# Kernel tuning notes

Hardware: AMD Instinct MI355X
Metric: run time of the kernel (lower is better)

## Reference

```python
import jax, jax.numpy as jnp
import numpy as np

# dimensions
N = 50000    # nodes
E = 600000   # edges
NS = 64      # scalar (0e) channels of node features
NV = 32      # vector (1o) channels of node features
A = 16       # node attr channels (16x0e)
R = 8        # edge embedding dim (radial basis, 8x0e)
H = 8        # fc_hidden_size
AVG_NB = 12.0  # avg_num_neighbors
# gate layout: NS scalars (silu) + NV gate scalars (sigmoid) gating NV vectors
GS = NS + NV  # 96 scalar channels before gate
NW = NS + NS + NV + NV  # 192 per-edge TP weights (paths: s*Y0->0e, s*Y1->1o, v*Y0->1o, v.Y1->0e)


def setup_inputs() -> dict:
    key = jax.random.key(0)
    ks = jax.random.split(key, 20)
    d = {
        'node_s': jax.random.normal(ks[0], (N, NS), jnp.float32),
        'node_v': jax.random.normal(ks[1], (N, NV, 3), jnp.float32),
        'node_attrs': jax.random.normal(ks[2], (N, A), jnp.float32),
        'edge_emb': jax.random.uniform(ks[3], (E, R), jnp.float32),
        'edge_sh0': jnp.ones((E, 1), jnp.float32),
        'edge_sh1': jax.random.normal(ks[4], (E, 3), jnp.float32),
        'edge_index': jax.random.randint(ks[5], (2, E), 0, N),
        # linear_1 on node feats (per-irrep channel mixing)
        'W1s': jax.random.normal(ks[6], (NS, NS), jnp.float32),
        'W1v': jax.random.normal(ks[7], (NV, NV), jnp.float32),
        # radial MLP producing per-edge TP weights
        'Wm1': jax.random.normal(ks[8], (R, H), jnp.float32),
        'Wm2': jax.random.normal(ks[9], (H, NW), jnp.float32),
        # linear_2: TP out (96x0e+96x1o) -> pre-gate (96x0e+32x1o)
        'W2s': jax.random.normal(ks[10], (GS, GS), jnp.float32),
        'W2v': jax.random.normal(ks[11], (NS + NV, NV), jnp.float32),
        # update UVU TP internal weights (msg x attrs)
        'Wt0': jax.random.normal(ks[12], (NS, A), jnp.float32),
        'Wt1': jax.random.normal(ks[13], (NV, A), jnp.float32),
        # linear_3
        'W3s': jax.random.normal(ks[14], (NS, GS), jnp.float32),
        'W3v': jax.random.normal(ks[15], (NV, NV), jnp.float32),
        # self connection: FullyConnectedTensorProduct(node_feats, attrs -> pre-gate)
        'Wsc0': jax.random.normal(ks[16], (NS, A, GS), jnp.float32),
        'Wsc1': jax.random.normal(ks[17], (NV, A, NV), jnp.float32),
    }
    return d


def _gate(s_all, v):
    # s_all: [.., GS]; first NS scalars -> silu, last NV -> sigmoid gates for vectors
    scal = jax.nn.silu(s_all[..., :NS])
    gates = jax.nn.sigmoid(s_all[..., NS:])
    return scal, v * gates[..., None]


def reference(node_s, node_v, node_attrs, edge_emb, edge_sh0, edge_sh1, edge_index,
              W1s, W1v, Wm1, Wm2, W2s, W2v, Wt0, Wt1, W3s, W3v, Wsc0, Wsc1):
    src, dst = edge_index[0], edge_index[1]

    # ---- message ----
    s1 = (node_s @ W1s) / jnp.sqrt(jnp.float32(NS))                       # [N,NS]
    v1 = jnp.einsum('nuc,uv->nvc', node_v, W1v) / jnp.sqrt(jnp.float32(NV))
    ss = s1[src]   # [E,NS]
    vv = v1[src]   # [E,NV,3]

    # per-edge TP weights from radial MLP
    w = jax.nn.silu(edge_emb @ Wm1) @ Wm2                                 # [E,NW]
    w0a, w1a, w1b, w0b = jnp.split(w, [NS, 2 * NS, 2 * NS + NV], axis=1)

    # UVU tensor product with SH edge attrs (lmax=1)
    t0a = w0a * ss * edge_sh0                                             # [E,NS] 0e
    t0b = w0b * jnp.einsum('euc,ec->eu', vv, edge_sh1)                    # [E,NV] 0e
    t1a = w1a[:, :, None] * ss[:, :, None] * edge_sh1[:, None, :]         # [E,NS,3] 1o
    t1b = w1b[:, :, None] * vv * edge_sh0[:, :, None]                     # [E,NV,3] 1o
    tp_s = jnp.concatenate([t0a, t0b], axis=1)                            # [E,96]
    tp_v = jnp.concatenate([t1a, t1b], axis=1)                            # [E,96,3]

    m_s = (tp_s @ W2s) / jnp.sqrt(jnp.float32(GS))                        # [E,GS]
    m_v = jnp.einsum('euc,uv->evc', tp_v, W2v) / jnp.sqrt(jnp.float32(NS + NV))  # [E,NV,3]
    msg_s, msg_v = _gate(m_s, m_v)                                        # [E,NS], [E,NV,3]

    # ---- update ----
    agg_s = jax.ops.segment_sum(msg_s, dst, num_segments=N) / jnp.sqrt(jnp.float32(AVG_NB))
    agg_v = jax.ops.segment_sum(msg_v, dst, num_segments=N) / jnp.sqrt(jnp.float32(AVG_NB))

    u0 = jnp.einsum('nu,na,ua->nu', agg_s, node_attrs, Wt0) / jnp.sqrt(jnp.float32(A))
    u1 = jnp.einsum('nuc,na,ua->nuc', agg_v, node_attrs, Wt1) / jnp.sqrt(jnp.float32(A))

    f_s = (u0 @ W3s) / jnp.sqrt(jnp.float32(NS))                          # [N,GS]
    f_v = jnp.einsum('nuc,uv->nvc', u1, W3v) / jnp.sqrt(jnp.float32(NV))  # [N,NV,3]

    # self connection (fully connected TP with scalar attrs)
    sc_s = jnp.einsum('nu,na,uav->nv', node_s, node_attrs, Wsc0) / jnp.sqrt(jnp.float32(NS * A))
    sc_v = jnp.einsum('nuc,na,uaw->nwc', node_v, node_attrs, Wsc1) / jnp.sqrt(jnp.float32(NV * A))
    f_s = f_s + sc_s
    f_v = f_v + sc_v

    out_s, out_v = _gate(f_s, f_v)                                        # [N,NS], [N,NV,3]
    return jnp.concatenate([out_s, out_v.reshape(N, NV * 3)], axis=1)     # [N,160]
```

## Files before the change

kernel.cpp:

```cpp
#include <hip/hip_runtime.h>
#include <math.h>

#define N 50000
#define E 600000
#define EPB 16
#define LDK 104

typedef __attribute__((ext_vector_type(8))) short short8;
typedef __attribute__((ext_vector_type(4))) float float4v;

__device__ __forceinline__ float silu_f(float x) { return x / (1.f + __expf(-x)); }
__device__ __forceinline__ float sigm_f(float x) { return 1.f / (1.f + __expf(-x)); }
__device__ __forceinline__ unsigned short f2bf(float f) {
  unsigned u = __float_as_uint(f);
  u += 0x7fff + ((u >> 16) & 1);
  return (unsigned short)(u >> 16);
}
__device__ __forceinline__ float bf2f(unsigned short u) {
  return __uint_as_float(((unsigned)u) << 16);
}

__global__ void k_hist(const int* __restrict__ eidx, int* __restrict__ counts) {
  int e = blockIdx.x * 256 + threadIdx.x;
  if (e < E) atomicAdd(&counts[eidx[E + e]], 1);
}

__global__ __launch_bounds__(1024)
void k_scan(const int* __restrict__ counts, int* __restrict__ row_ptr) {
  __shared__ int ssum[1024];
  const int t = threadIdx.x;
  const int CH = 49;
  int lo = t * CH, hi = min(lo + CH, N);
  int s = 0;
  for (int i = lo; i < hi; i++) s += counts[i];
  ssum[t] = s;
  __syncthreads();
  for (int off = 1; off < 1024; off <<= 1) {
    int v = (t >= off) ? ssum[t - off] : 0;
    __syncthreads();
    ssum[t] += v;
    __syncthreads();
  }
  int run = (t == 0) ? 0 : ssum[t - 1];
  for (int i = lo; i < hi; i++) { row_ptr[i] = run; run += counts[i]; }
  if (t == 1023) row_ptr[N] = ssum[1023];
}

__global__ void k_scatter(const int* __restrict__ eidx, const int* __restrict__ row_ptr,
                          int* __restrict__ woff, int* __restrict__ perm) {
  int e = blockIdx.x * 256 + threadIdx.x;
  if (e < E) {
    int d = eidx[E + e];
    int p = atomicAdd(&woff[d], 1);
    perm[row_ptr[d] + p] = e;
  }
}

__global__ void k_prep(const float* __restrict__ Wsc0, const float* __restrict__ W3s,
                       const float* __restrict__ Wsc1, const float* __restrict__ W3v,
                       const float* __restrict__ W2s, const float* __restrict__ W2v,
                       unsigned short* __restrict__ BT, unsigned short* __restrict__ B2T,
                       unsigned short* __restrict__ w2sTg, unsigned short* __restrict__ w2vTg) {
  const float isq96 = 0.10206207261596575f;
  int i = blockIdx.x * 256 + threadIdx.x;
  if (i < 96 * 1088) {
    int j = i / 1088, k = i % 1088;
    float v;
    if (k < 1024) v = Wsc0[(size_t)k * 96 + j] * 0.03125f;
    else          v = W3s[(size_t)(k - 1024) * 96 + j] * 0.125f;
    BT[i] = f2bf(v);
  } else if (i < 96 * 1088 + 32 * 576) {
    int i2 = i - 96 * 1088;
    int w = i2 / 576, k = i2 % 576;
    float v = 0.f;
    if (k < 512)      v = Wsc1[(size_t)k * 32 + w] * 0.04419417382415922f;
    else if (k < 544) v = W3v[(size_t)(k - 512) * 32 + w] * 0.17677669529663689f;
    B2T[i2] = f2bf(v);
  } else if (i < 96 * 1088 + 32 * 576 + 96 * 96) {
    int i3 = i - (96 * 1088 + 32 * 576);
    int j = i3 / 96, k = i3 % 96;
    w2sTg[i3] = f2bf(W2s[(size_t)k * 96 + j] * isq96);
  } else {
    int i4 = i - (96 * 1088 + 32 * 576 + 96 * 96);
    if (i4 < 32 * 96) {
      int v = i4 / 96, u = i4 % 96;
      w2vTg[i4] = f2bf(W2v[(size_t)u * 32 + v] * isq96);
    }
  }
}

__global__ __launch_bounds__(256, 4)
void k_lin1(const float* __restrict__ node_s, const float* __restrict__ node_v,
            const float* __restrict__ W1s, const float* __restrict__ W1v,
            float* __restrict__ s1, float* __restrict__ v1) {
  __shared__ float w1s[64 * 64];
  __shared__ float w1v[32 * 32];
  for (int i = threadIdx.x; i < 64 * 64; i += 256) w1s[i] = W1s[i];
  for (int i = threadIdx.x; i < 32 * 32; i += 256) w1v[i] = W1v[i];
  __syncthreads();
  const float is_ns = 0.125f;
  const float is_nv = 0.17677669529663689f;
  int gtid = blockIdx.x * 256 + threadIdx.x;
  int stride = gridDim.x * 256;
  for (int i = gtid; i < N * 160; i += stride) {
    int n = i / 160, ch = i % 160;
    if (ch < 64) {
      const float* row = node_s + n * 64;
      float acc = 0.f;
#pragma unroll
      for (int u = 0; u < 64; u++) acc += row[u] * w1s[u * 64 + ch];
      s1[n * 64 + ch] = acc * is_ns;
    } else {
      int p = ch - 64, v = p / 3, c = p % 3;
      const float* row = node_v + n * 96;
      float acc = 0.f;
#pragma unroll
      for (int u = 0; u < 32; u++) acc += row[u * 3 + c] * w1v[u * 32 + v];
      v1[n * 96 + p] = acc * is_nv;
    }
  }
}

template<int STORE>
__global__ __launch_bounds__(256, 4)
void k_msg(const float* __restrict__ s1, const float* __restrict__ v1,
           const float* __restrict__ emb, const float* __restrict__ sh0g,
           const float* __restrict__ sh1g, const int* __restrict__ eidx,
           const int* __restrict__ perm,
           const float* __restrict__ Wm1, const float* __restrict__ Wm2,
           const unsigned short* __restrict__ w2sTg, const unsigned short* __restrict__ w2vTg,
           float* __restrict__ aggs, float* __restrict__ aggv,
           unsigned short* __restrict__ msgS, unsigned short* __restrict__ msgV) {
  __shared__ float wm2s[192 * 9];
  __shared__ float wm1s[64];
  __shared__ unsigned short tps[EPB * LDK];
  __shared__ unsigned short tpv[EPB * 3 * LDK];
  __shared__ float gat[EPB][33];
  __shared__ float hb[EPB][8];
  __shared__ float sh1b[EPB][4];
  __shared__ float sh0b[EPB];
  __shared__ int ssrc[EPB];
  __shared__ int sdst[EPB];

  const int t = threadIdx.x;
  const int wave = t >> 6, lane = t & 63;
  const int lm = lane & 15, quad = lane >> 4;
  const int subc = t & 15;

  for (int i = t; i < 192 * 8; i += 256) {
    int h = i / 192, c = i % 192;
    wm2s[c * 9 + h] = Wm2[i];
  }
  if (t < 64) wm1s[t] = Wm1[t];

  short8 b1fr[2][3], b2fr[3];
  {
    const int nt0 = wave;
    const int nt1 = (wave + 4 < 6) ? wave + 4 : wave;
    const int nv2 = wave & 1;
#pragma unroll
    for (int kk = 0; kk < 3; kk++) {
      b1fr[0][kk] = *(const short8*)&w2sTg[(nt0 * 16 + lm) * 96 + kk * 32 + quad * 8];
      b1fr[1][kk] = *(const short8*)&w2sTg[(nt1 * 16 + lm) * 96 + kk * 32 + quad * 8];
      b2fr[kk]    = *(const short8*)&w2vTg[(nv2 * 16 + lm) * 96 + kk * 32 + quad * 8];
    }
  }
  __syncthreads();

  for (int pass = blockIdx.x; pass < E / EPB; pass += gridDim.x) {
    const int ebase = pass * EPB;
    __syncthreads();
    if (t < EPB) {
      const int e = STORE ? perm[ebase + t] : (ebase + t);
      ssrc[t] = eidx[e];
      if (!STORE) sdst[t] = eidx[E + ebase + t];
      sh0b[t] = sh0g[e];
    } else if (t >= 64 && t < 64 + EPB * 3) {
      int i = t - 64;
      const int el = i / 3, c = i % 3;
      const int e = STORE ? perm[ebase + el] : (ebase + el);
      sh1b[el][c] = sh1g[e * 3 + c];
    } else if (t >= 128) {
      int i = t - 128, el = i >> 3, sub = i & 7;
      const int e = STORE ? perm[ebase + el] : (ebase + el);
      float acc = 0.f;
#pragma unroll
      for (int r = 0; r < 8; r++) acc += emb[e * 8 + r] * wm1s[r * 8 + sub];
      hb[el][sub] = silu_f(acc);
    }
    __syncthreads();
    {
      const int el = t >> 4, sub = subc;
      const int src = ssrc[el];
      const float s0v = sh0b[el];
      const float x0 = sh1b[el][0], x1 = sh1b[el][1], x2 = sh1b[el][2];
      float hr[8];
#pragma unroll
      for (int h = 0; h < 8; h++) hr[h] = hb[el][h];
      const float4v ss = *(const float4v*)&s1[(size_t)src * 64 + sub * 4];
      unsigned short tsv[4], tvv[3][4];
#pragma unroll
      for (int i = 0; i < 4; i++) {
        float w0a = 0.f, w1a = 0.f;
#pragma unroll
        for (int h = 0; h < 8; h++) {
          w0a += hr[h] * wm2s[(sub * 4 + i) * 9 + h];
          w1a += hr[h] * wm2s[(64 + sub * 4 + i) * 9 + h];
        }
        const float ssu = ss[i];
        tsv[i] = f2bf(w0a * ssu * s0v);
        const float base = w1a * ssu;
        tvv[0][i] = f2bf(base * x0);
        tvv[1][i] = f2bf(base * x1);
        tvv[2][i] = f2bf(base * x2);
      }
      *(uint2*)&tps[el * LDK + sub * 4] = *(uint2*)tsv;
#pragma unroll
      for (int c = 0; c < 3; c++)
        *(uint2*)&tpv[(el * 3 + c) * LDK + sub * 4] = *(uint2*)tvv[c];
      const float2* vp = (const float2*)&v1[(size_t)src * 96 + sub * 6];
      const float2 va = vp[0], vb = vp[1], vc = vp[2];
      const float v6[6] = {va.x, va.y, vb.x, vb.y, vc.x, vc.y};
      unsigned short ts2[2], tv2[3][2];
#pragma unroll
      for (int i2 = 0; i2 < 2; i2++) {
        float w1b = 0.f, w0b = 0.f;
#pragma unroll
        for (int h = 0; h < 8; h++) {
          w1b += hr[h] * wm2s[(128 + sub * 2 + i2) * 9 + h];
          w0b += hr[h] * wm2s[(160 + sub * 2 + i2) * 9 + h];
        }
        const float vx = v6[i2 * 3 + 0], vy = v6[i2 * 3 + 1], vz = v6[i2 * 3 + 2];
        ts2[i2] = f2bf(w0b * (vx * x0 + vy * x1 + vz * x2));
        tv2[0][i2] = f2bf(w1b * vx * s0v);
        tv2[1][i2] = f2bf(w1b * vy * s0v);
        tv2[2][i2] = f2bf(w1b * vz * s0v);
      }
      *(unsigned*)&tps[el * LDK + 64 + sub * 2] = *(unsigned*)ts2;
#pragma unroll
      for (int c = 0; c < 3; c++)
        *(unsigned*)&tpv[(el * 3 + c) * LDK + 64 + sub * 2] = *(unsigned*)tv2[c];
    }
    __syncthreads();
    {
      short8 afr[3];
#pragma unroll
      for (int kk = 0; kk < 3; kk++)
        afr[kk] = *(const short8*)&tps[lm * LDK + kk * 32 + quad * 8];
#pragma unroll
      for (int t2 = 0; t2 < 2; t2++) {
        const int nt = wave + t2 * 4;
        if (nt < 6) {
          float4v acc = {0.f, 0.f, 0.f, 0.f};
#pragma unroll
          for (int kk = 0; kk < 3; kk++)
            acc = __builtin_amdgcn_mfma_f32_16x16x32_bf16(afr[kk], b1fr[t2][kk], acc, 0, 0, 0);
          const int j = nt * 16 + lm;
#pragma unroll
          for (int reg = 0; reg < 4; reg++) {
            const int e = quad * 4 + reg;
            const float val = acc[reg];
            if (j < 64) {
              if (STORE) msgS[(size_t)(ebase + e) * 64 + j] = f2bf(silu_f(val));
              else atomicAdd(&aggs[(size_t)sdst[e] * 64 + j], silu_f(val));
            } else {
              gat[e][j - 64] = sigm_f(val);
            }
          }
        }
      }
    }
    __syncthreads();
#pragma unroll
    for (int t2 = 0; t2 < 2; t2++) {
      const int tile = wave + t2 * 4;
      if (tile < 6) {
        const int mt = tile >> 1, nt2 = tile & 1;
        float4v acc = {0.f, 0.f, 0.f, 0.f};
#pragma unroll
        for (int kk = 0; kk < 3; kk++) {
          short8 a = *(const short8*)&tpv[(mt * 16 + lm) * LDK + kk * 32 + quad * 8];
          acc = __builtin_amdgcn_mfma_f32_16x16x32_bf16(a, b2fr[kk], acc, 0, 0, 0);
        }
        const int v = nt2 * 16 + lm;
#pragma unroll
        for (int reg = 0; reg < 4; reg++) {
          const int r = mt * 16 + quad * 4 + reg;
          const int e = (r * 171) >> 9, c = r - 3 * e;
          const float val = acc[reg] * gat[e][v];
          if (STORE) msgV[(size_t)(ebase + e) * 96 + v * 3 + c] = f2bf(val);
          else atomicAdd(&aggv[(size_t)sdst[e] * 96 + v * 3 + c], val);
        }
      }
    }
  }
}

__global__ __launch_bounds__(256, 8)
void k_agg(const unsigned short* __restrict__ msgS, const unsigned short* __restrict__ msgV,
           const int* __restrict__ rowp,
           float* __restrict__ aggs, float* __restrict__ aggv) {
  const int wv = threadIdx.x >> 6, lane = threadIdx.x & 63;
  const int n = blockIdx.x * 4 + wv;
  const int lo = rowp[n], hi = rowp[n + 1];
  float sS = 0.f, v0 = 0.f, v1a = 0.f;
  int r = lo;
  for (; r + 2 <= hi; r += 2) {
    const unsigned short a0 = msgS[(size_t)r * 64 + lane];
    const unsigned short a1 = msgS[(size_t)(r + 1) * 64 + lane];
    const unsigned short b0 = msgV[(size_t)r * 96 + lane];
    const unsigned short b1 = msgV[(size_t)(r + 1) * 96 + lane];
    unsigned short c0 = 0, c1 = 0;
    if (lane < 32) {
      c0 = msgV[(size_t)r * 96 + 64 + lane];
      c1 = msgV[(size_t)(r + 1) * 96 + 64 + lane];
    }
    sS += bf2f(a0) + bf2f(a1);
    v0 += bf2f(b0) + bf2f(b1);
    v1a += bf2f(c0) + bf2f(c1);
  }
  for (; r < hi; r++) {
    sS += bf2f(msgS[(size_t)r * 64 + lane]);
    v0 += bf2f(msgV[(size_t)r * 96 + lane]);
    if (lane < 32) v1a += bf2f(msgV[(size_t)r * 96 + 64 + lane]);
  }
  aggs[(size_t)n * 64 + lane] = sS;
  aggv[(size_t)n * 96 + lane] = v0;
  if (lane < 32) aggv[(size_t)n * 96 + 64 + lane] = v1a;
}

__global__ __launch_bounds__(256, 4)
void k_c1(const float* __restrict__ node_s, const float* __restrict__ attrs,
          const float* __restrict__ aggs, const float* __restrict__ Wt0,
          const unsigned short* __restrict__ BT,
          float* __restrict__ out, float* __restrict__ gates) {
  __shared__ float s_row[32][64];
  __shared__ float attr[32][16];
  __shared__ float t0[32][64];
  __shared__ float wt0[1024];
  __shared__ unsigned short As[32 * 72];
  const int t = threadIdx.x;
  const int wave = t >> 6, lane = t & 63, lm = lane & 15, quad = lane >> 4;
  const int nbase = blockIdx.x * 32;

  for (int i = t; i < 1024; i += 256) wt0[i] = Wt0[i];
  for (int i = t; i < 2048; i += 256) {
    int nl = i >> 6, u = i & 63, n = nbase + nl;
    s_row[nl][u] = (n < N) ? node_s[(size_t)n * 64 + u] : 0.f;
    t0[nl][u]    = (n < N) ? aggs[(size_t)n * 64 + u] : 0.f;
  }
  for (int i = t; i < 512; i += 256) {
    int nl = i >> 4, a = i & 15, n = nbase + nl;
    attr[nl][a] = (n < N) ? attrs[(size_t)n * 16 + a] : 0.f;
  }
  __syncthreads();
  for (int i = t; i < 2048; i += 256) {
    int nl = i >> 6, u = i & 63;
    float d0 = 0.f;
#pragma unroll
    for (int a = 0; a < 16; a++) d0 += attr[nl][a] * wt0[u * 16 + a];
    t0[nl][u] *= d0 * 0.07216878364870322f;
  }

  float4v acc[3] = {{0,0,0,0},{0,0,0,0},{0,0,0,0}};
  int mts[3], nts[3];
#pragma unroll
  for (int tt = 0; tt < 3; tt++) {
    const int tile = wave + tt * 4;
    mts[tt] = tile / 6;
    nts[tt] = tile % 6;
  }

  for (int kc = 0; kc < 17; kc++) {
    __syncthreads();
    {
      const int row = t >> 3, c0 = (t & 7) * 8;
      unsigned short tmp[8];
      if (kc < 16) {
        const int u = kc * 4 + (c0 >> 4);
        const float sval = s_row[row][u];
        const int ab = c0 & 8;
#pragma unroll
        for (int i = 0; i < 8; i++) tmp[i] = f2bf(sval * attr[row][ab + i]);
      } else {
#pragma unroll
        for (int i = 0; i < 8; i++) tmp[i] = f2bf(t0[row][c0 + i]);
      }
      *(uint4*)&As[row * 72 + c0] = *(uint4*)tmp;
    }
    __syncthreads();
#pragma unroll
    for (int ks = 0; ks < 2; ks++) {
      short8 am0 = *(const short8*)&As[(lm) * 72 + ks * 32 + quad * 8];
      short8 am1 = *(const short8*)&As[(16 + lm) * 72 + ks * 32 + quad * 8];
#pragma unroll
      for (int tt = 0; tt < 3; tt++) {
        short8 b = *(const short8*)&BT[(size_t)(nts[tt] * 16 + lm) * 1088 + kc * 64 + ks * 32 + quad * 8];
        acc[tt] = __builtin_amdgcn_mfma_f32_16x16x32_bf16(mts[tt] ? am1 : am0, b, acc[tt], 0, 0, 0);
      }
    }
  }
#pragma unroll
  for (int tt = 0; tt < 3; tt++) {
    const int j = nts[tt] * 16 + lm;
#pragma unroll
    for (int reg = 0; reg < 4; reg++) {
      const int m = mts[tt] * 16 + quad * 4 + reg;
      const int n = nbase + m;
      if (n < N) {
        const float val = acc[tt][reg];
        if (j < 64) out[(size_t)n * 160 + j] = silu_f(val);
        else        gates[(size_t)n * 32 + (j - 64)] = sigm_f(val);
      }
    }
  }
}

__global__ __launch_bounds__(256, 3)
void k_c2(const float* __restrict__ node_v, const float* __restrict__ attrs,
          const float* __restrict__ aggv, const float* __restrict__ Wt1,
          const unsigned short* __restrict__ B2T, const float* __restrict__ gts,
          float* __restrict__ out) {
  __shared__ float nvs[32][96];
  __shared__ float t1s[32][96];
  __shared__ float attr[32][16];
  __shared__ float wt1[512];
  __shared__ unsigned short As2[96 * 72];
  const int t = threadIdx.x;
  const int wave = t >> 6, lane = t & 63, lm = lane & 15, quad = lane >> 4;
  const int nbase = blockIdx.x * 32;

  for (int i = t; i < 512; i += 256) wt1[i] = Wt1[i];
  for (int i = t; i < 32 * 96; i += 256) {
    int nl = i / 96, rr = i % 96, n = nbase + nl;
    nvs[nl][rr] = (n < N) ? node_v[(size_t)n * 96 + rr] : 0.f;
    t1s[nl][rr] = (n < N) ? aggv[(size_t)n * 96 + rr] : 0.f;
  }
  for (int i = t; i < 512; i += 256) {
    int nl = i >> 4, a = i & 15, n = nbase + nl;
    attr[nl][a] = (n < N) ? attrs[(size_t)n * 16 + a] : 0.f;
  }
  __syncthreads();
  for (int i = t; i < 1024; i += 256) {
    int nl = i >> 5, u = i & 31;
    float d1 = 0.f;
#pragma unroll
    for (int a = 0; a < 16; a++) d1 += attr[nl][a] * wt1[u * 16 + a];
    d1 *= 0.07216878364870322f;
    t1s[nl][u * 3 + 0] *= d1; t1s[nl][u * 3 + 1] *= d1; t1s[nl][u * 3 + 2] *= d1;
  }

  float4v acc[3] = {{0,0,0,0},{0,0,0,0},{0,0,0,0}};
  int mts[3], nts[3];
#pragma unroll
  for (int tt = 0; tt < 3; tt++) {
    const int tile = wave + tt * 4;
    mts[tt] = tile >> 1;
    nts[tt] = tile & 1;
  }

  for (int kc = 0; kc < 9; kc++) {
    __syncthreads();
#pragma unroll
    for (int jj = 0; jj < 3; jj++) {
      const int job = t + jj * 256;
      const int row = job >> 3, c0 = (job & 7) * 8;
      const int nl = (row * 171) >> 9, c = row - 3 * nl;
      const int kbase = kc * 64 + c0;
      unsigned short tmp[8];
      if (kbase < 512) {
        const int u = kbase >> 4;
        const float vval = nvs[nl][u * 3 + c];
        const int ab = c0 & 8;
#pragma unroll
        for (int i = 0; i < 8; i++) tmp[i] = f2bf(vval * attr[nl][ab + i]);
      } else if (kbase < 544) {
        const int u2 = kbase - 512;
#pragma unroll
        for (int i = 0; i < 8; i++) tmp[i] = f2bf(t1s[nl][(u2 + i) * 3 + c]);
      } else {
#pragma unroll
        for (int i = 0; i < 8; i++) tmp[i] = 0;
      }
      *(uint4*)&As2[row * 72 + c0] = *(uint4*)tmp;
    }
    __syncthreads();
#pragma unroll
    for (int ks = 0; ks < 2; ks++) {
#pragma unroll
      for (int tt = 0; tt < 3; tt++) {
        short8 a = *(const short8*)&As2[(mts[tt] * 16 + lm) * 72 + ks * 32 + quad * 8];
        short8 b = *(const short8*)&B2T[(size_t)(nts[tt] * 16 + lm) * 576 + kc * 64 + ks * 32 + quad * 8];
        acc[tt] = __builtin_amdgcn_mfma_f32_16x16x32_bf16(a, b, acc[tt], 0, 0, 0);
      }
    }
  }
#pragma unroll
  for (int tt = 0; tt < 3; tt++) {
    const int w = nts[tt] * 16 + lm;
#pragma unroll
    for (int reg = 0; reg < 4; reg++) {
      const int row = mts[tt] * 16 + quad * 4 + reg;
      const int nl = (row * 171) >> 9, c = row - 3 * nl;
      const int n = nbase + nl;
      if (n < N)
        out[(size_t)n * 160 + 64 + w * 3 + c] = acc[tt][reg] * gts[(size_t)n * 32 + w];
    }
  }
}

extern "C" void kernel_launch(void* const* d_in, const int* in_sizes, int n_in,
                              void* d_out, int out_size, void* d_ws, size_t ws_size,
                              hipStream_t stream) {
  const float* node_s = (const float*)d_in[0];
  const float* node_v = (const float*)d_in[1];
  const float* attrs  = (const float*)d_in[2];
  const float* emb    = (const float*)d_in[3];
  const float* sh0    = (const float*)d_in[4];
  const float* sh1    = (const float*)d_in[5];
  const int*   eidx   = (const int*)d_in[6];
  const float* W1s    = (const float*)d_in[7];
  const float* W1v    = (const float*)d_in[8];
  const float* Wm1    = (const float*)d_in[9];
  const float* Wm2    = (const float*)d_in[10];
  const float* W2s    = (const float*)d_in[11];
  const float* W2v    = (const float*)d_in[12];
  const float* Wt0    = (const float*)d_in[13];
  const float* Wt1    = (const float*)d_in[14];
  const float* W3s    = (const float*)d_in[15];
  const float* W3v    = (const float*)d_in[16];
  const float* Wsc0   = (const float*)d_in[17];
  const float* Wsc1   = (const float*)d_in[18];

  char* p = (char*)d_ws;
  float* s1  = (float*)p;  p += (size_t)N * 64 * 4;
  float* v1f = (float*)p;  p += (size_t)N * 96 * 4;
  float* gts = (float*)p;  p += (size_t)N * 32 * 4;
  unsigned short* BT    = (unsigned short*)p;  p += (size_t)96 * 1088 * 2;
  unsigned short* B2T   = (unsigned short*)p;  p += (size_t)32 * 576 * 2;
  unsigned short* w2sTg = (unsigned short*)p;  p += (size_t)96 * 96 * 2;
  unsigned short* w2vTg = (unsigned short*)p;  p += (size_t)32 * 96 * 2;
  char* pmode = p;
  size_t base = (size_t)(pmode - (char*)d_ws);
  size_t need_store = base + ((size_t)N + 1) * 4 + (size_t)N * 4 + (size_t)N * 4
                    + (size_t)E * 4 + (size_t)E * 64 * 2 + (size_t)E * 96 * 2;
  const bool store = (ws_size >= need_store);

  k_prep<<<528, 256, 0, stream>>>(Wsc0, W3s, Wsc1, W3v, W2s, W2v, BT, B2T, w2sTg, w2vTg);
  k_lin1<<<1024, 256, 0, stream>>>(node_s, node_v, W1s, W1v, s1, v1f);

  if (store) {
    int* rowp = (int*)pmode;
    int* cnt  = rowp + (N + 1);
    int* woff = cnt + N;
    int* perm = woff + N;
    unsigned short* msgS = (unsigned short*)(perm + E);
    unsigned short* msgV = msgS + (size_t)E * 64;
    hipMemsetAsync(cnt, 0, (size_t)N * 2 * 4, stream);
    k_hist<<<(E + 255) / 256, 256, 0, stream>>>(eidx, cnt);
    k_scan<<<1, 1024, 0, stream>>>(cnt, rowp);
    k_scatter<<<(E + 255) / 256, 256, 0, stream>>>(eidx, rowp, woff, perm);
    k_msg<1><<<1024, 256, 0, stream>>>(s1, v1f, emb, sh0, sh1, eidx, perm, Wm1, Wm2,
                                       w2sTg, w2vTg, nullptr, nullptr, msgS, msgV);
    float* aggs = s1;
    float* aggv = v1f;
    k_agg<<<N / 4, 256, 0, stream>>>(msgS, msgV, rowp, aggs, aggv);
    k_c1<<<1563, 256, 0, stream>>>(node_s, attrs, aggs, Wt0, BT, (float*)d_out, gts);
    k_c2<<<1563, 256, 0, stream>>>(node_v, attrs, aggv, Wt1, B2T, gts, (float*)d_out);
  } else {
    float* aggs = (float*)pmode;
    float* aggv = aggs + (size_t)N * 64;
    hipMemsetAsync(aggs, 0, (size_t)N * 160 * 4, stream);
    k_msg<0><<<1024, 256, 0, stream>>>(s1, v1f, emb, sh0, sh1, eidx, nullptr, Wm1, Wm2,
                                       w2sTg, w2vTg, aggs, aggv, nullptr, nullptr);
    k_c1<<<1563, 256, 0, stream>>>(node_s, attrs, aggs, Wt0, BT, (float*)d_out, gts);
    k_c2<<<1563, 256, 0, stream>>>(node_v, attrs, aggv, Wt1, B2T, gts, (float*)d_out);
  }
}
```

Measured before the change: 740.4 us.

## Fuse segmented per-destination reduction into message kernel, drop bf16 message buffer

The sorted-by-destination path no longer writes per-edge bf16 messages to global memory for a separate gather-sum kernel. Each block instead stages its 16 sorted edges' messages in shared memory and does a run-length segmented sum by destination, issuing one fp32 atomic per run per channel into zeroed aggregation buffers. This removes the large per-edge message write and reread (E×160 bf16) and one kernel launch. In exchange it adds an extra memset, a block barrier, and atomics that still run about once per edge per channel, since average degree is close to the block's edge count. It also adds shared-memory usage that may reduce occupancy.

```diff
diff --git a/kernel.cpp b/kernel.cpp
--- a/kernel.cpp
+++ b/kernel.cpp
@@ -129,13 +129,14 @@
            const int* __restrict__ perm,
            const float* __restrict__ Wm1, const float* __restrict__ Wm2,
            const unsigned short* __restrict__ w2sTg, const unsigned short* __restrict__ w2vTg,
-           float* __restrict__ aggs, float* __restrict__ aggv,
-           unsigned short* __restrict__ msgS, unsigned short* __restrict__ msgV) {
+           float* __restrict__ aggs, float* __restrict__ aggv) {
   __shared__ float wm2s[192 * 9];
   __shared__ float wm1s[64];
   __shared__ unsigned short tps[EPB * LDK];
   __shared__ unsigned short tpv[EPB * 3 * LDK];
   __shared__ float gat[EPB][33];
+  __shared__ float msL[EPB][65];
+  __shared__ float mvL[EPB][97];
   __shared__ float hb[EPB][8];
   __shared__ float sh1b[EPB][4];
   __shared__ float sh0b[EPB];
@@ -173,7 +174,7 @@
     if (t < EPB) {
       const int e = STORE ? perm[ebase + t] : (ebase + t);
       ssrc[t] = eidx[e];
-      if (!STORE) sdst[t] = eidx[E + ebase + t];
+      sdst[t] = eidx[E + e];
       sh0b[t] = sh0g[e];
     } else if (t >= 64 && t < 64 + EPB * 3) {
       int i = t - 64;
@@ -261,7 +262,7 @@
             const int e = quad * 4 + reg;
             const float val = acc[reg];
             if (j < 64) {
-              if (STORE) msgS[(size_t)(ebase + e) * 64 + j] = f2bf(silu_f(val));
+              if (STORE) msL[e][j] = silu_f(val);
               else atomicAdd(&aggs[(size_t)sdst[e] * 64 + j], silu_f(val));
             } else {
               gat[e][j - 64] = sigm_f(val);
@@ -288,45 +289,31 @@
           const int r = mt * 16 + quad * 4 + reg;
           const int e = (r * 171) >> 9, c = r - 3 * e;
           const float val = acc[reg] * gat[e][v];
-          if (STORE) msgV[(size_t)(ebase + e) * 96 + v * 3 + c] = f2bf(val);
+          if (STORE) mvL[e][v * 3 + c] = val;
           else atomicAdd(&aggv[(size_t)sdst[e] * 96 + v * 3 + c], val);
         }
       }
     }
-  }
-}
-
-__global__ __launch_bounds__(256, 8)
-void k_agg(const unsigned short* __restrict__ msgS, const unsigned short* __restrict__ msgV,
-           const int* __restrict__ rowp,
-           float* __restrict__ aggs, float* __restrict__ aggv) {
-  const int wv = threadIdx.x >> 6, lane = threadIdx.x & 63;
-  const int n = blockIdx.x * 4 + wv;
-  const int lo = rowp[n], hi = rowp[n + 1];
-  float sS = 0.f, v0 = 0.f, v1a = 0.f;
-  int r = lo;
-  for (; r + 2 <= hi; r += 2) {
-    const unsigned short a0 = msgS[(size_t)r * 64 + lane];
-    const unsigned short a1 = msgS[(size_t)(r + 1) * 64 + lane];
-    const unsigned short b0 = msgV[(size_t)r * 96 + lane];
-    const unsigned short b1 = msgV[(size_t)(r + 1) * 96 + lane];
-    unsigned short c0 = 0, c1 = 0;
-    if (lane < 32) {
-      c0 = msgV[(size_t)r * 96 + 64 + lane];
-      c1 = msgV[(size_t)(r + 1) * 96 + 64 + lane];
-    }
-    sS += bf2f(a0) + bf2f(a1);
-    v0 += bf2f(b0) + bf2f(b1);
-    v1a += bf2f(c0) + bf2f(c1);
-  }
-  for (; r < hi; r++) {
-    sS += bf2f(msgS[(size_t)r * 64 + lane]);
-    v0 += bf2f(msgV[(size_t)r * 96 + lane]);
-    if (lane < 32) v1a += bf2f(msgV[(size_t)r * 96 + 64 + lane]);
-  }
-  aggs[(size_t)n * 64 + lane] = sS;
-  aggv[(size_t)n * 96 + lane] = v0;
-  if (lane < 32) aggv[(size_t)n * 96 + 64 + lane] = v1a;
+    if (STORE) {
+      __syncthreads();
+      if (t < 160) {
+        float acc = 0.f;
+        int cur = sdst[0];
+        for (int s2 = 0; s2 < EPB; s2++) {
+          const int d = sdst[s2];
+          const float val = (t < 64) ? msL[s2][t] : mvL[s2][t - 64];
+          if (d != cur) {
+            if (t < 64) atomicAdd(&aggs[(size_t)cur * 64 + t], acc);
+            else        atomicAdd(&aggv[(size_t)cur * 96 + (t - 64)], acc);
+            acc = 0.f; cur = d;
+          }
+          acc += val;
+        }
+        if (t < 64) atomicAdd(&aggs[(size_t)cur * 64 + t], acc);
+        else        atomicAdd(&aggv[(size_t)cur * 96 + (t - 64)], acc);
+      }
+    }
+  }
 }
 
 __global__ __launch_bounds__(256, 4)
@@ -543,7 +530,7 @@
   char* pmode = p;
   size_t base = (size_t)(pmode - (char*)d_ws);
   size_t need_store = base + ((size_t)N + 1) * 4 + (size_t)N * 4 + (size_t)N * 4
-                    + (size_t)E * 4 + (size_t)E * 64 * 2 + (size_t)E * 96 * 2;
+                    + (size_t)E * 4 + (size_t)N * 160 * 4;
   const bool store = (ws_size >= need_store);
 
   k_prep<<<528, 256, 0, stream>>>(Wsc0, W3s, Wsc1, W3v, W2s, W2v, BT, B2T, w2sTg, w2vTg);
@@ -554,17 +541,15 @@
     int* cnt  = rowp + (N + 1);
     int* woff = cnt + N;
     int* perm = woff + N;
-    unsigned short* msgS = (unsigned short*)(perm + E);
-    unsigned short* msgV = msgS + (size_t)E * 64;
+    float* aggs = (float*)(perm + E);
+    float* aggv = aggs + (size_t)N * 64;
     hipMemsetAsync(cnt, 0, (size_t)N * 2 * 4, stream);
+    hipMemsetAsync(aggs, 0, (size_t)N * 160 * 4, stream);
     k_hist<<<(E + 255) / 256, 256, 0, stream>>>(eidx, cnt);
     k_scan<<<1, 1024, 0, stream>>>(cnt, rowp);
     k_scatter<<<(E + 255) / 256, 256, 0, stream>>>(eidx, rowp, woff, perm);
     k_msg<1><<<1024, 256, 0, stream>>>(s1, v1f, emb, sh0, sh1, eidx, perm, Wm1, Wm2,
-                                       w2sTg, w2vTg, nullptr, nullptr, msgS, msgV);
-    float* aggs = s1;
-    float* aggv = v1f;
-    k_agg<<<N / 4, 256, 0, stream>>>(msgS, msgV, rowp, aggs, aggv);
+                                       w2sTg, w2vTg, aggs, aggv);
     k_c1<<<1563, 256, 0, stream>>>(node_s, attrs, aggs, Wt0, BT, (float*)d_out, gts);
     k_c2<<<1563, 256, 0, stream>>>(node_v, attrs, aggv, Wt1, B2T, gts, (float*)d_out);
   } else {
@@ -572,7 +557,7 @@
     float* aggv = aggs + (size_t)N * 64;
     hipMemsetAsync(aggs, 0, (size_t)N * 160 * 4, stream);
     k_msg<0><<<1024, 256, 0, stream>>>(s1, v1f, emb, sh0, sh1, eidx, nullptr, Wm1, Wm2,
-                                       w2sTg, w2vTg, aggs, aggv, nullptr, nullptr);
+                                       w2sTg, w2vTg, aggs, aggv);
     k_c1<<<1563, 256, 0, stream>>>(node_s, attrs, aggs, Wt0, BT, (float*)d_out, gts);
     k_c2<<<1563, 256, 0, stream>>>(node_v, attrs, aggv, Wt1, B2T, gts, (float*)d_out);
   }
```

New measurement: 716.1 us. 1.03x faster.
